# Performance work log

Measured on AMD Instinct MI355X. Metric: run time of the kernel, lower is better.

The kernel has to match this reference:

```python
import jax, jax.numpy as jnp
import numpy as np

B, L, INPUT_DIM = 4, 4096, 32
D_MODEL, N_LAYERS = 256, 2
D_STATE, D_CONV, EXPAND = 16, 4, 2
D_INNER = EXPAND * D_MODEL          # 512
DT_RANK = (D_MODEL + 15) // 16      # 16
OUTPUT_DIM, HORIZON = 32, 4
LN_EPS = 1e-5


def setup_inputs() -> dict:
    key = jax.random.key(0)
    ks = jax.random.split(key, 16)
    s = 0.02
    inp = {
        "x": jax.random.normal(ks[0], (B, L, INPUT_DIM), jnp.float32),
        "enc_w": jax.random.normal(ks[1], (D_MODEL, INPUT_DIM), jnp.float32) * s,
        "enc_b": jnp.zeros((D_MODEL,), jnp.float32),
        "in_proj_w": jax.random.normal(ks[2], (N_LAYERS, 2 * D_INNER, D_MODEL), jnp.float32) * s,
        "conv_w": jax.random.normal(ks[3], (N_LAYERS, D_INNER, D_CONV), jnp.float32) * s,
        "conv_b": jnp.zeros((N_LAYERS, D_INNER), jnp.float32),
        "xproj_w": jax.random.normal(ks[4], (N_LAYERS, DT_RANK + 2 * D_STATE, D_INNER), jnp.float32) * s,
        "dtproj_w": jax.random.normal(ks[5], (N_LAYERS, D_INNER, DT_RANK), jnp.float32) * s,
        "dtproj_b": jax.random.normal(ks[6], (N_LAYERS, D_INNER), jnp.float32) * 0.1,
        "A_log": jnp.log(jnp.tile(jnp.arange(1.0, D_STATE + 1.0, dtype=jnp.float32), (N_LAYERS, D_INNER, 1))),
        "Dp": jnp.ones((N_LAYERS, D_INNER), jnp.float32),
        "out_proj_w": jax.random.normal(ks[7], (N_LAYERS, D_MODEL, D_INNER), jnp.float32) * s,
        "ln_g": jnp.ones((D_MODEL,), jnp.float32),
        "ln_b": jnp.zeros((D_MODEL,), jnp.float32),
        "head_w": jax.random.normal(ks[8], (OUTPUT_DIM * HORIZON, D_MODEL), jnp.float32) * s,
        "head_b": jnp.zeros((OUTPUT_DIM * HORIZON,), jnp.float32),
    }
    return inp


def _mamba_block(x, in_w, cw, cb, xp_w, dt_w, dt_b, A_log, Dp, out_w):
    # x: [B, L, d_model]
    b, l, _ = x.shape
    xz = jnp.einsum("bld,ed->ble", x, in_w)            # [B, L, 2*d_inner]
    xi, res = jnp.split(xz, 2, axis=-1)
    # causal depthwise conv1d (padding=d_conv-1, truncated to L)
    xpad = jnp.pad(xi, ((0, 0), (D_CONV - 1, 0), (0, 0)))
    xi = sum(xpad[:, k:k + l, :] * cw[:, k] for k in range(D_CONV)) + cb
    xi = jax.nn.silu(xi)
    dbl = jnp.einsum("bld,ed->ble", xi, xp_w)           # [B, L, dt_rank+2*d_state]
    dt = dbl[..., :DT_RANK]
    Bm = dbl[..., DT_RANK:DT_RANK + D_STATE]            # [B, L, d_state]
    Cm = dbl[..., DT_RANK + D_STATE:]                   # [B, L, d_state]
    dt = jax.nn.softplus(jnp.einsum("blr,dr->bld", dt, dt_w) + dt_b)  # [B, L, d_inner]
    A = -jnp.exp(A_log)                                 # [d_inner, d_state]

    def step(h, ins):
        dt_t, B_t, C_t, x_t = ins                       # [B,di],[B,ds],[B,ds],[B,di]
        dA = jnp.exp(dt_t[..., None] * A)               # [B, d_inner, d_state]
        h = dA * h + (dt_t * x_t)[..., None] * B_t[:, None, :]
        y = jnp.einsum("bds,bs->bd", h, C_t)
        return h, y

    h0 = jnp.zeros((b, D_INNER, D_STATE), x.dtype)
    xs = (jnp.moveaxis(dt, 1, 0), jnp.moveaxis(Bm, 1, 0),
          jnp.moveaxis(Cm, 1, 0), jnp.moveaxis(xi, 1, 0))
    _, ys = jax.lax.scan(step, h0, xs)                  # ys: [L, B, d_inner]
    y = jnp.moveaxis(ys, 0, 1) + xi * Dp
    y = y * jax.nn.silu(res)
    return jnp.einsum("ble,de->bld", y, out_w)


def reference(x, enc_w, enc_b, in_proj_w, conv_w, conv_b, xproj_w, dtproj_w,
              dtproj_b, A_log, Dp, out_proj_w, ln_g, ln_b, head_w, head_b):
    h = jnp.einsum("bli,di->bld", x, enc_w) + enc_b     # encoder
    for i in range(N_LAYERS):
        h = h + _mamba_block(h, in_proj_w[i], conv_w[i], conv_b[i], xproj_w[i],
                             dtproj_w[i], dtproj_b[i], A_log[i], Dp[i], out_proj_w[i])
    mu = jnp.mean(h, axis=-1, keepdims=True)
    var = jnp.mean((h - mu) ** 2, axis=-1, keepdims=True)
    hn = (h - mu) * jax.lax.rsqrt(var + LN_EPS) * ln_g + ln_b
    state = hn[:, -1, :]                                # last timestep
    return jnp.einsum("bd,od->bo", state, head_w) + head_b
```

## Files before the change

### kernel.cpp

```cpp
#include <hip/hip_runtime.h>
#include <hip/hip_bf16.h>
#include <math.h>

#define BB 4
#define LL 4096
#define DM 256
#define DI 512
#define DS 16
#define NOUTK 128
#define LN_EPS 1e-5f
#define NC 128
#define CLEN (LL/NC)
#define BL (BB*LL)
#define LDB 640

typedef __attribute__((ext_vector_type(8))) short short8;
typedef __attribute__((ext_vector_type(4))) float f32x4;

__device__ __forceinline__ ushort f2bf(float f) {
    union { float f; unsigned u; } v; v.f = f;
    unsigned r = (v.u + 0x7FFF + ((v.u >> 16) & 1)) >> 16;
    return (ushort)r;
}
__device__ __forceinline__ float bf2f(ushort u) {
    union { unsigned u; float f; } v; v.u = ((unsigned)u) << 16;
    return v.f;
}

__global__ __launch_bounds__(256) void cast_bf16_kernel(
    const float* __restrict__ src, ushort* __restrict__ dst, int n)
{
    int i = blockIdx.x * 256 + threadIdx.x;
    if (i < n) dst[i] = f2bf(src[i]);
}

__global__ __launch_bounds__(256) void build_comb_kernel(
    const float* __restrict__ xpw, const float* __restrict__ dtw,
    ushort* __restrict__ dst)
{
    int i = blockIdx.x * 256 + threadIdx.x;
    int l = i / (640 * 512);
    int rem = i - l * 640 * 512;
    int row = rem >> 9, k = rem & 511;
    const float* xp = xpw + l * 48 * 512;
    const float* dw = dtw + l * 512 * 16;
    float v;
    if (row < 512) {
        v = 0.f;
        #pragma unroll
        for (int r = 0; r < 16; ++r)
            v = fmaf(dw[row * 16 + r], xp[r * 512 + k], v);
    } else if (row < 544) {
        v = xp[(row - 512 + 16) * 512 + k];
    } else v = 0.f;
    dst[i] = f2bf(v);
}

__global__ __launch_bounds__(256) void enc_kernel(
    const float* __restrict__ x, const float* __restrict__ w,
    const float* __restrict__ b, float* __restrict__ h,
    ushort* __restrict__ hbf)
{
    __shared__ float sw[256 * 33];
    __shared__ float sx[4][32];
    int tid = threadIdx.x;
    for (int i = tid; i < 256 * 8; i += 256) {
        float4 v = ((const float4*)w)[i];
        int r = i >> 3, c = (i & 7) * 4;
        sw[r * 33 + c + 0] = v.x; sw[r * 33 + c + 1] = v.y;
        sw[r * 33 + c + 2] = v.z; sw[r * 33 + c + 3] = v.w;
    }
    int row0 = blockIdx.x * 4;
    if (tid < 32) {
        for (int rr = 0; rr < 4; ++rr)
            sx[rr][tid] = x[(size_t)(row0 + rr) * 32 + tid];
    }
    __syncthreads();
    float bb = b[tid];
    #pragma unroll
    for (int rr = 0; rr < 4; ++rr) {
        float acc = bb;
        #pragma unroll
        for (int k = 0; k < 32; ++k)
            acc = fmaf(sx[rr][k], sw[tid * 33 + k], acc);
        size_t o = (size_t)(row0 + rr) * DM + tid;
        h[o] = acc;
        hbf[o] = f2bf(acc);
    }
}

template<int EPI, bool F32OUT, bool RESID, bool BF16OUT>
__global__ __launch_bounds__(256) void mfma_gemm(
    const ushort* __restrict__ A, int lda,
    const ushort* __restrict__ W,
    const float* __restrict__ bias,
    float* __restrict__ C, int ldc,
    ushort* __restrict__ Cbf, int ldcbf,
    int K)
{
    __shared__ ushort As[2][128 * 64];
    __shared__ ushort Ws[2][128 * 64];
    const int tid = threadIdx.x;

    int nwg = gridDim.x * gridDim.y;
    int wlin = blockIdx.y * gridDim.x + blockIdx.x;
    int gx = blockIdx.x, gy = blockIdx.y;
    if ((nwg & 7) == 0) {
        int q = nwg >> 3;
        int s = (wlin & 7) * q + (wlin >> 3);
        gx = s % gridDim.x;
        gy = s / gridDim.x;
    }
    const int bm = gy * 128;
    const int bn = gx * 128;
    const int wid = tid >> 6, lane = tid & 63;
    const int wrow = (wid >> 1) * 64, wcol = (wid & 1) * 64;
    const int sr = tid >> 3;
    const int sc = tid & 7;

    f32x4 acc[4][4];
    #pragma unroll
    for (int mi = 0; mi < 4; ++mi)
        #pragma unroll
        for (int ni = 0; ni < 4; ++ni)
            acc[mi][ni] = (f32x4){0.f, 0.f, 0.f, 0.f};

#define STAGE(b, k0) do {                                                     \
    _Pragma("unroll")                                                         \
    for (int it = 0; it < 4; ++it) {                                          \
        int r = it * 32 + sr;                                                 \
        int csrc = sc ^ (r & 7);                                              \
        __builtin_amdgcn_global_load_lds(                                     \
            (const __attribute__((address_space(1))) unsigned int*)           \
                (A + (size_t)(bm + r) * lda + (k0) + csrc * 8),               \
            (__attribute__((address_space(3))) unsigned int*)                 \
                (&As[b][r * 64 + sc * 8]), 16, 0, 0);                         \
    }                                                                         \
    _Pragma("unroll")                                                         \
    for (int it = 0; it < 4; ++it) {                                          \
        int r = it * 32 + sr;                                                 \
        int csrc = sc ^ (r & 7);                                              \
        __builtin_amdgcn_global_load_lds(                                     \
            (const __attribute__((address_space(1))) unsigned int*)           \
                (W + (size_t)(bn + r) * K + (k0) + csrc * 8),                 \
            (__attribute__((address_space(3))) unsigned int*)                 \
                (&Ws[b][r * 64 + sc * 8]), 16, 0, 0);                         \
    }                                                                         \
} while (0)

#define COMPUTE(b) do {                                                       \
    _Pragma("unroll")                                                         \
    for (int kk = 0; kk < 2; ++kk) {                                          \
        short8 af[4], bfr[4];                                                 \
        _Pragma("unroll")                                                     \
        for (int mi = 0; mi < 4; ++mi) {                                      \
            int r = wrow + mi * 16 + (lane & 15);                             \
            int c = (lane >> 4) + kk * 4;                                     \
            af[mi] = *(const short8*)(&As[b][r * 64 + ((c ^ (r & 7)) << 3)]); \
        }                                                                     \
        _Pragma("unroll")                                                     \
        for (int ni = 0; ni < 4; ++ni) {                                      \
            int r = wcol + ni * 16 + (lane & 15);                             \
            int c = (lane >> 4) + kk * 4;                                     \
            bfr[ni] = *(const short8*)(&Ws[b][r * 64 + ((c ^ (r & 7)) << 3)]);\
        }                                                                     \
        _Pragma("unroll")                                                     \
        for (int mi = 0; mi < 4; ++mi)                                        \
            _Pragma("unroll")                                                 \
            for (int ni = 0; ni < 4; ++ni)                                    \
                acc[mi][ni] = __builtin_amdgcn_mfma_f32_16x16x32_bf16(        \
                    af[mi], bfr[ni], acc[mi][ni], 0, 0, 0);                   \
    }                                                                         \
} while (0)

    const int nk = K >> 6;
    STAGE(0, 0);
    for (int t = 0; t < nk; t += 2) {
        __syncthreads();
        if (t + 1 < nk) STAGE(1, (t + 1) << 6);
        COMPUTE(0);
        __syncthreads();
        if (t + 2 < nk) STAGE(0, (t + 2) << 6);
        COMPUTE(1);
    }
#undef STAGE
#undef COMPUTE

    #pragma unroll
    for (int mi = 0; mi < 4; ++mi)
        #pragma unroll
        for (int ni = 0; ni < 4; ++ni) {
            int col = bn + wcol + ni * 16 + (lane & 15);
            #pragma unroll
            for (int r = 0; r < 4; ++r) {
                int row = bm + wrow + mi * 16 + (lane >> 4) * 4 + r;
                float v = acc[mi][ni][r];
                if (EPI == 1) {
                    if (col < 512) {
                        float u = v + bias[col];
                        float sp = fmaxf(u, 0.f) + __logf(1.f + __expf(-fabsf(u)));
                        Cbf[(size_t)row * ldcbf + col] = f2bf(sp);
                    } else if (col < 544) {
                        C[(size_t)row * ldc + (col - 512)] = v;
                    }
                } else {
                    if (F32OUT) {
                        float* cp = C + (size_t)row * ldc + col;
                        float vv = v;
                        if (RESID) vv += *cp;
                        *cp = vv;
                        if (BF16OUT) Cbf[(size_t)row * ldcbf + col] = f2bf(vv);
                    } else if (BF16OUT) {
                        Cbf[(size_t)row * ldcbf + col] = f2bf(v);
                    }
                }
            }
        }
}

__global__ __launch_bounds__(256) void conv_silu_kernel(
    const ushort* __restrict__ xz, const float* __restrict__ cw,
    const float* __restrict__ cb, ushort* __restrict__ xi)
{
    int idx = blockIdx.x * 256 + threadIdx.x;
    int d4 = (idx & 127) * 4;
    int bt = idx >> 7;
    int t = bt & (LL - 1);
    const ushort* base = xz + (size_t)bt * 1024 + d4;
    float acc[4];
    float4 w[4];
    #pragma unroll
    for (int j = 0; j < 4; ++j) {
        acc[j] = cb[d4 + j];
        w[j] = *(const float4*)(cw + (d4 + j) * 4);
    }
    #pragma unroll
    for (int k = 0; k < 4; ++k) {
        int back = 3 - k;
        if (t >= back) {
            ushort4 v = *(const ushort4*)(base - back * 1024);
            float wk0 = (k==0)?w[0].x:(k==1)?w[0].y:(k==2)?w[0].z:w[0].w;
            float wk1 = (k==0)?w[1].x:(k==1)?w[1].y:(k==2)?w[1].z:w[1].w;
            float wk2 = (k==0)?w[2].x:(k==1)?w[2].y:(k==2)?w[2].z:w[2].w;
            float wk3 = (k==0)?w[3].x:(k==1)?w[3].y:(k==2)?w[3].z:w[3].w;
            acc[0] = fmaf(bf2f(v.x), wk0, acc[0]);
            acc[1] = fmaf(bf2f(v.y), wk1, acc[1]);
            acc[2] = fmaf(bf2f(v.z), wk2, acc[2]);
            acc[3] = fmaf(bf2f(v.w), wk3, acc[3]);
        }
    }
    ushort4 o;
    float s0 = acc[0] / (1.f + __expf(-acc[0]));
    float s1 = acc[1] / (1.f + __expf(-acc[1]));
    float s2 = acc[2] / (1.f + __expf(-acc[2]));
    float s3 = acc[3] / (1.f + __expf(-acc[3]));
    o.x = f2bf(s0); o.y = f2bf(s1); o.z = f2bf(s2); o.w = f2bf(s3);
    *(ushort4*)(xi + (size_t)bt * 512 + d4) = o;
}

__global__ __launch_bounds__(256) void scan_phase1(
    const ushort* __restrict__ xi, const ushort* __restrict__ dtb,
    const float* __restrict__ bc,
    const float* __restrict__ alog,
    float* __restrict__ cA, float* __restrict__ cH)
{
    int d = blockIdx.z * 256 + threadIdx.x;
    int b = blockIdx.y, c = blockIdx.x;
    float Av[16];
    bool fast = true;
    #pragma unroll
    for (int s = 0; s < 16; ++s) {
        Av[s] = -__expf(alog[d * 16 + s]);
        fast = fast && (fabsf(Av[s] + (float)(s + 1)) < 1e-3f * (s + 1));
    }
    float h[16], P[16];
    #pragma unroll
    for (int s = 0; s < 16; ++s) { h[s] = 0.f; P[s] = 1.f; }
    int t0 = c * CLEN;
    if (fast) {
        float Pe = 1.f;
        for (int t = t0; t < t0 + CLEN; ++t) {
            size_t row = (size_t)b * LL + t;
            float dt = bf2f(dtb[row * 512 + d]);
            float x = bf2f(xi[row * 512 + d]);
            float dtx = dt * x;
            const float* bp = bc + row * 32;
            float e1 = __expf(-dt);
            float e2=e1*e1, e3=e2*e1, e4=e2*e2, e5=e3*e2, e6=e3*e3, e7=e4*e3, e8=e4*e4;
            float e9=e5*e4, e10=e5*e5, e11=e6*e5, e12=e6*e6, e13=e7*e6, e14=e7*e7, e15=e8*e7, e16=e8*e8;
            float pw[16] = {e1,e2,e3,e4,e5,e6,e7,e8,e9,e10,e11,e12,e13,e14,e15,e16};
            #pragma unroll
            for (int s = 0; s < 16; ++s)
                h[s] = fmaf(pw[s], h[s], dtx * bp[s]);
            Pe *= e1;
        }
        float p1=Pe, p2=p1*p1, p3=p2*p1, p4=p2*p2, p5=p3*p2, p6=p3*p3, p7=p4*p3, p8=p4*p4;
        float p9=p5*p4, p10=p5*p5, p11=p6*p5, p12=p6*p6, p13=p7*p6, p14=p7*p7, p15=p8*p7, p16=p8*p8;
        float pp[16] = {p1,p2,p3,p4,p5,p6,p7,p8,p9,p10,p11,p12,p13,p14,p15,p16};
        #pragma unroll
        for (int s = 0; s < 16; ++s) P[s] = pp[s];
    } else {
        for (int t = t0; t < t0 + CLEN; ++t) {
            size_t row = (size_t)b * LL + t;
            float dt = bf2f(dtb[row * 512 + d]);
            float x = bf2f(xi[row * 512 + d]);
            float dtx = dt * x;
            const float* bp = bc + row * 32;
            #pragma unroll
            for (int s = 0; s < 16; ++s) {
                float dA = __expf(dt * Av[s]);
                h[s] = fmaf(dA, h[s], dtx * bp[s]);
                P[s] *= dA;
            }
        }
    }
    size_t base = (((size_t)b * DI + d) * NC + c) * 16;
    #pragma unroll
    for (int q = 0; q < 4; ++q) {
        *(float4*)(cA + base + q*4) = *(float4*)&P[q*4];
        *(float4*)(cH + base + q*4) = *(float4*)&h[q*4];
    }
}

__global__ __launch_bounds__(256) void scan_phase2(
    const float* __restrict__ cA, float* __restrict__ cH)
{
    int idx = blockIdx.x * 256 + threadIdx.x;
    int s = idx & 15;
    int bd = idx >> 4;
    size_t base = (size_t)bd * NC * 16 + s;
    float init = 0.f;
    for (int c = 0; c < NC; ++c) {
        size_t o = base + (size_t)c * 16;
        float a = cA[o], hh = cH[o];
        cH[o] = init;
        init = fmaf(a, init, hh);
    }
}

__global__ __launch_bounds__(256) void scan_phase3(
    const ushort* __restrict__ xz,
    ushort* __restrict__ xi,
    const ushort* __restrict__ dtb,
    const float* __restrict__ bc,
    const float* __restrict__ alog,
    const float* __restrict__ Dp,
    const float* __restrict__ cH,
    int c0)
{
    int d = blockIdx.z * 256 + threadIdx.x;
    int b = blockIdx.y;
    int c = blockIdx.x + c0;
    float Av[16];
    bool fast = true;
    #pragma unroll
    for (int s = 0; s < 16; ++s) {
        Av[s] = -__expf(alog[d * 16 + s]);
        fast = fast && (fabsf(Av[s] + (float)(s + 1)) < 1e-3f * (s + 1));
    }
    float h[16];
    size_t cbase = (((size_t)b * DI + d) * NC + c) * 16;
    #pragma unroll
    for (int q = 0; q < 4; ++q)
        *(float4*)&h[q*4] = *(const float4*)(cH + cbase + q*4);
    float Dd = Dp[d];
    int t0 = c * CLEN;
    if (fast) {
        for (int t = t0; t < t0 + CLEN; ++t) {
            size_t row = (size_t)b * LL + t;
            float dt = bf2f(dtb[row * 512 + d]);
            float x = bf2f(xi[row * 512 + d]);
            float dtx = dt * x;
            const float* bp = bc + row * 32;
            const float* cp = bc + row * 32 + 16;
            float e1 = __expf(-dt);
            float e2=e1*e1, e3=e2*e1, e4=e2*e2, e5=e3*e2, e6=e3*e3, e7=e4*e3, e8=e4*e4;
            float e9=e5*e4, e10=e5*e5, e11=e6*e5, e12=e6*e6, e13=e7*e6, e14=e7*e7, e15=e8*e7, e16=e8*e8;
            float pw[16] = {e1,e2,e3,e4,e5,e6,e7,e8,e9,e10,e11,e12,e13,e14,e15,e16};
            float y = 0.f;
            #pragma unroll
            for (int s = 0; s < 16; ++s) {
                h[s] = fmaf(pw[s], h[s], dtx * bp[s]);
                y = fmaf(h[s], cp[s], y);
            }
            float res = bf2f(xz[row * 1024 + 512 + d]);
            float g = (y + x * Dd) * (res / (1.f + __expf(-res)));
            xi[row * 512 + d] = f2bf(g);
        }
    } else {
        for (int t = t0; t < t0 + CLEN; ++t) {
            size_t row = (size_t)b * LL + t;
            float dt = bf2f(dtb[row * 512 + d]);
            float x = bf2f(xi[row * 512 + d]);
            float dtx = dt * x;
            const float* bp = bc + row * 32;
            const float* cp = bc + row * 32 + 16;
            float y = 0.f;
            #pragma unroll
            for (int s = 0; s < 16; ++s) {
                float dA = __expf(dt * Av[s]);
                h[s] = fmaf(dA, h[s], dtx * bp[s]);
                y = fmaf(h[s], cp[s], y);
            }
            float res = bf2f(xz[row * 1024 + 512 + d]);
            float g = (y + x * Dd) * (res / (1.f + __expf(-res)));
            xi[row * 512 + d] = f2bf(g);
        }
    }
}

__global__ __launch_bounds__(256) void out_proj_last_kernel(
    const ushort* __restrict__ xi, const float* __restrict__ W,
    float* __restrict__ h)
{
    int b = blockIdx.x, n = threadIdx.x;
    __shared__ float sy[DI];
    const ushort* yrow = xi + ((size_t)b * LL + (LL - 1)) * DI;
    for (int k = threadIdx.x; k < DI; k += 256) sy[k] = bf2f(yrow[k]);
    __syncthreads();
    const float* wr = W + (size_t)n * DI;
    float acc = 0.f;
    for (int k = 0; k < DI; k += 4) {
        float4 wv = *(const float4*)(wr + k);
        acc = fmaf(sy[k+0], wv.x, acc);
        acc = fmaf(sy[k+1], wv.y, acc);
        acc = fmaf(sy[k+2], wv.z, acc);
        acc = fmaf(sy[k+3], wv.w, acc);
    }
    h[((size_t)b * LL + (LL - 1)) * DM + n] += acc;
}

__global__ __launch_bounds__(256) void ln_head_kernel(
    const float* __restrict__ h, const float* __restrict__ lng,
    const float* __restrict__ lnb, const float* __restrict__ hw,
    const float* __restrict__ hb, float* __restrict__ out)
{
    int b = blockIdx.x, tid = threadIdx.x;
    __shared__ float sh[DM];
    __shared__ float r1[4], r2[4];
    float v = h[((size_t)b * LL + (LL - 1)) * DM + tid];
    float s = v;
    #pragma unroll
    for (int o = 32; o >= 1; o >>= 1) s += __shfl_down(s, o);
    if ((tid & 63) == 0) r1[tid >> 6] = s;
    __syncthreads();
    float mu = (r1[0] + r1[1] + r1[2] + r1[3]) * (1.f / 256.f);
    float dv = v - mu;
    float q = dv * dv;
    #pragma unroll
    for (int o = 32; o >= 1; o >>= 1) q += __shfl_down(q, o);
    if ((tid & 63) == 0) r2[tid >> 6] = q;
    __syncthreads();
    float var = (r2[0] + r2[1] + r2[2] + r2[3]) * (1.f / 256.f);
    sh[tid] = dv * rsqrtf(var + LN_EPS) * lng[tid] + lnb[tid];
    __syncthreads();
    if (tid < NOUTK) {
        const float* wr = hw + (size_t)tid * DM;
        float acc = hb[tid];
        for (int d2 = 0; d2 < DM; d2 += 4) {
            float4 wv = *(const float4*)(wr + d2);
            acc = fmaf(sh[d2+0], wv.x, acc);
            acc = fmaf(sh[d2+1], wv.y, acc);
            acc = fmaf(sh[d2+2], wv.z, acc);
            acc = fmaf(sh[d2+3], wv.w, acc);
        }
        out[b * NOUTK + tid] = acc;
    }
}

extern "C" void kernel_launch(void* const* d_in, const int* in_sizes, int n_in,
                              void* d_out, int out_size, void* d_ws, size_t ws_size,
                              hipStream_t stream)
{
    const float* x    = (const float*)d_in[0];
    const float* encw = (const float*)d_in[1];
    const float* encb = (const float*)d_in[2];
    const float* inw  = (const float*)d_in[3];
    const float* cw   = (const float*)d_in[4];
    const float* cb   = (const float*)d_in[5];
    const float* xpw  = (const float*)d_in[6];
    const float* dtw  = (const float*)d_in[7];
    const float* dtb  = (const float*)d_in[8];
    const float* alog = (const float*)d_in[9];
    const float* Dp   = (const float*)d_in[10];
    const float* opw  = (const float*)d_in[11];
    const float* lng  = (const float*)d_in[12];
    const float* lnb  = (const float*)d_in[13];
    const float* hw   = (const float*)d_in[14];
    const float* hb   = (const float*)d_in[15];
    float* out = (float*)d_out;

    float* ws   = (float*)d_ws;
    float* h    = ws;
    float* bc   = h   + (size_t)BL * DM;
    float* cA   = bc  + (size_t)BL * 32;
    float* cH   = cA  + (size_t)BB * DI * NC * DS;
    ushort* h_bf    = (ushort*)(cH + (size_t)BB * DI * NC * DS);
    ushort* xz_bf   = h_bf  + (size_t)BL * DM;
    ushort* xi_bf   = xz_bf + (size_t)BL * 1024;
    ushort* dt_bf   = xi_bf + (size_t)BL * DI;
    ushort* inw_bf  = dt_bf + (size_t)BL * DI;
    ushort* opw_bf  = inw_bf + 2 * 1024 * DM;
    ushort* comb_bf = opw_bf + 2 * DM * DI;

    dim3 blk(256, 1, 1);

    cast_bf16_kernel<<<dim3((2*1024*DM)/256), blk, 0, stream>>>(inw, inw_bf, 2*1024*DM);
    cast_bf16_kernel<<<dim3((2*DM*DI)/256), blk, 0, stream>>>(opw, opw_bf, 2*DM*DI);
    build_comb_kernel<<<dim3((2*640*512)/256), blk, 0, stream>>>(xpw, dtw, comb_bf);

    enc_kernel<<<dim3(BL/4), blk, 0, stream>>>(x, encw, encb, h, h_bf);

    for (int l = 0; l < 2; ++l) {
        mfma_gemm<0,false,false,true><<<dim3(1024/128, BL/128), blk, 0, stream>>>(
            h_bf, DM, inw_bf + (size_t)l * 1024 * DM, nullptr,
            nullptr, 0, xz_bf, 1024, DM);
        conv_silu_kernel<<<dim3(BL * 128 / 256), blk, 0, stream>>>(
            xz_bf, cw + l * DI * 4, cb + l * DI, xi_bf);
        mfma_gemm<1,false,false,false><<<dim3(LDB/128, BL/128), blk, 0, stream>>>(
            xi_bf, DI, comb_bf + (size_t)l * LDB * DI, dtb + l * DI,
            bc, 32, dt_bf, 512, DI);
        scan_phase1<<<dim3(NC, BB, 2), blk, 0, stream>>>(
            xi_bf, dt_bf, bc, alog + (size_t)l * DI * 16, cA, cH);
        scan_phase2<<<dim3(BB * DI * DS / 256), blk, 0, stream>>>(cA, cH);
        if (l == 0) {
            scan_phase3<<<dim3(NC, BB, 2), blk, 0, stream>>>(
                xz_bf, xi_bf, dt_bf, bc, alog + (size_t)l * DI * 16,
                Dp + l * DI, cH, 0);
            mfma_gemm<0,true,true,true><<<dim3(DM/128, BL/128), blk, 0, stream>>>(
                xi_bf, DI, opw_bf + (size_t)l * DM * DI, nullptr,
                h, DM, h_bf, DM, DI);
        } else {
            scan_phase3<<<dim3(1, BB, 2), blk, 0, stream>>>(
                xz_bf, xi_bf, dt_bf, bc, alog + (size_t)l * DI * 16,
                Dp + l * DI, cH, NC - 1);
            out_proj_last_kernel<<<dim3(BB), blk, 0, stream>>>(
                xi_bf, opw + (size_t)l * DM * DI, h);
        }
    }

    ln_head_kernel<<<dim3(BB), blk, 0, stream>>>(h, lng, lnb, hw, hb, out);
}
```

Measured before the change: 375.1 us.

## Shrink GEMM M-tile, single-barrier prefetch pipeline, parallelize scan phase2

The MFMA GEMM M-tile drops from 128 to 64 rows, and the kernel gets launch bounds for four waves per SIMD, so there are twice as many workgroups and higher occupancy. The K loop now issues the next stage's global-to-LDS loads and waits with an explicit vmcnt rather than a full sync. scan_phase2 moves from one thread serially walking all 128 chunks per (b,d,s) to 16 threads per state, each combining 8 chunks, with a shuffle-based prefix scan across them. The trade-offs are less weight reuse per tile and a hand-written vmcnt count that must stay in step with the number of loads issued.

Result: no change. 375.0 us (-0.0%).

```diff
diff --git a/kernel.cpp b/kernel.cpp
--- a/kernel.cpp
+++ b/kernel.cpp
@@ -90,7 +90,7 @@
 }
 
 template<int EPI, bool F32OUT, bool RESID, bool BF16OUT>
-__global__ __launch_bounds__(256) void mfma_gemm(
+__global__ __launch_bounds__(256, 4) void mfma_gemm(
     const ushort* __restrict__ A, int lda,
     const ushort* __restrict__ W,
     const float* __restrict__ bias,
@@ -98,8 +98,8 @@
     ushort* __restrict__ Cbf, int ldcbf,
     int K)
 {
-    __shared__ ushort As[2][128 * 64];
-    __shared__ ushort Ws[2][128 * 64];
+    __shared__ __align__(16) ushort As[2][64 * 64];
+    __shared__ __align__(16) ushort Ws[2][128 * 64];
     const int tid = threadIdx.x;
 
     int nwg = gridDim.x * gridDim.y;
@@ -111,30 +111,30 @@
         gx = s % gridDim.x;
         gy = s / gridDim.x;
     }
-    const int bm = gy * 128;
+    const int bm = gy * 64;
     const int bn = gx * 128;
     const int wid = tid >> 6, lane = tid & 63;
-    const int wrow = (wid >> 1) * 64, wcol = (wid & 1) * 64;
+    const int wrow = (wid >> 1) * 32, wcol = (wid & 1) * 64;
     const int sr = tid >> 3;
     const int sc = tid & 7;
 
-    f32x4 acc[4][4];
-    #pragma unroll
-    for (int mi = 0; mi < 4; ++mi)
+    f32x4 acc[2][4];
+    #pragma unroll
+    for (int mi = 0; mi < 2; ++mi)
         #pragma unroll
         for (int ni = 0; ni < 4; ++ni)
             acc[mi][ni] = (f32x4){0.f, 0.f, 0.f, 0.f};
 
-#define STAGE(b, k0) do {                                                     \
+#define STAGE(buf, k0) do {                                                   \
     _Pragma("unroll")                                                         \
-    for (int it = 0; it < 4; ++it) {                                          \
+    for (int it = 0; it < 2; ++it) {                                          \
         int r = it * 32 + sr;                                                 \
         int csrc = sc ^ (r & 7);                                              \
         __builtin_amdgcn_global_load_lds(                                     \
             (const __attribute__((address_space(1))) unsigned int*)           \
                 (A + (size_t)(bm + r) * lda + (k0) + csrc * 8),               \
             (__attribute__((address_space(3))) unsigned int*)                 \
-                (&As[b][r * 64 + sc * 8]), 16, 0, 0);                         \
+                (&As[buf][r * 64 + sc * 8]), 16, 0, 0);                       \
     }                                                                         \
     _Pragma("unroll")                                                         \
     for (int it = 0; it < 4; ++it) {                                          \
@@ -144,28 +144,28 @@
             (const __attribute__((address_space(1))) unsigned int*)           \
                 (W + (size_t)(bn + r) * K + (k0) + csrc * 8),                 \
             (__attribute__((address_space(3))) unsigned int*)                 \
-                (&Ws[b][r * 64 + sc * 8]), 16, 0, 0);                         \
+                (&Ws[buf][r * 64 + sc * 8]), 16, 0, 0);                       \
     }                                                                         \
 } while (0)
 
-#define COMPUTE(b) do {                                                       \
+#define COMPUTE(buf) do {                                                     \
     _Pragma("unroll")                                                         \
     for (int kk = 0; kk < 2; ++kk) {                                          \
-        short8 af[4], bfr[4];                                                 \
+        short8 af[2], bfr[4];                                                 \
         _Pragma("unroll")                                                     \
-        for (int mi = 0; mi < 4; ++mi) {                                      \
+        for (int mi = 0; mi < 2; ++mi) {                                      \
             int r = wrow + mi * 16 + (lane & 15);                             \
             int c = (lane >> 4) + kk * 4;                                     \
-            af[mi] = *(const short8*)(&As[b][r * 64 + ((c ^ (r & 7)) << 3)]); \
+            af[mi] = *(const short8*)(&As[buf][r * 64 + ((c ^ (r & 7)) << 3)]);\
         }                                                                     \
         _Pragma("unroll")                                                     \
         for (int ni = 0; ni < 4; ++ni) {                                      \
             int r = wcol + ni * 16 + (lane & 15);                             \
             int c = (lane >> 4) + kk * 4;                                     \
-            bfr[ni] = *(const short8*)(&Ws[b][r * 64 + ((c ^ (r & 7)) << 3)]);\
+            bfr[ni] = *(const short8*)(&Ws[buf][r * 64 + ((c ^ (r & 7)) << 3)]);\
         }                                                                     \
         _Pragma("unroll")                                                     \
-        for (int mi = 0; mi < 4; ++mi)                                        \
+        for (int mi = 0; mi < 2; ++mi)                                        \
             _Pragma("unroll")                                                 \
             for (int ni = 0; ni < 4; ++ni)                                    \
                 acc[mi][ni] = __builtin_amdgcn_mfma_f32_16x16x32_bf16(        \
@@ -175,19 +175,24 @@
 
     const int nk = K >> 6;
     STAGE(0, 0);
-    for (int t = 0; t < nk; t += 2) {
-        __syncthreads();
-        if (t + 1 < nk) STAGE(1, (t + 1) << 6);
-        COMPUTE(0);
-        __syncthreads();
-        if (t + 2 < nk) STAGE(0, (t + 2) << 6);
-        COMPUTE(1);
+    for (int t = 0; t < nk; ++t) {
+        if (t + 1 < nk) {
+            STAGE((t + 1) & 1, (t + 1) << 6);
+            asm volatile("s_waitcnt vmcnt(6)" ::: "memory");
+        } else {
+            asm volatile("s_waitcnt vmcnt(0)" ::: "memory");
+        }
+        __builtin_amdgcn_s_barrier();
+        asm volatile("" ::: "memory");
+        COMPUTE(t & 1);
+        asm volatile("" ::: "memory");
+        __builtin_amdgcn_s_barrier();
     }
 #undef STAGE
 #undef COMPUTE
 
     #pragma unroll
-    for (int mi = 0; mi < 4; ++mi)
+    for (int mi = 0; mi < 2; ++mi)
         #pragma unroll
         for (int ni = 0; ni < 4; ++ni) {
             int col = bn + wcol + ni * 16 + (lane & 15);
@@ -325,16 +330,36 @@
 __global__ __launch_bounds__(256) void scan_phase2(
     const float* __restrict__ cA, float* __restrict__ cH)
 {
-    int idx = blockIdx.x * 256 + threadIdx.x;
-    int s = idx & 15;
-    int bd = idx >> 4;
+    int bd = blockIdx.x;
+    int tid = threadIdx.x;
+    int s = tid >> 4;
+    int g = tid & 15;
     size_t base = (size_t)bd * NC * 16 + s;
-    float init = 0.f;
-    for (int c = 0; c < NC; ++c) {
-        size_t o = base + (size_t)c * 16;
-        float a = cA[o], hh = cH[o];
+    float a8[8], h8[8];
+    #pragma unroll
+    for (int j = 0; j < 8; ++j) {
+        size_t o = base + (size_t)(g * 8 + j) * 16;
+        a8[j] = cA[o]; h8[j] = cH[o];
+    }
+    float A = 1.f, H = 0.f;
+    #pragma unroll
+    for (int j = 0; j < 8; ++j) {
+        H = fmaf(a8[j], H, h8[j]);
+        A *= a8[j];
+    }
+    #pragma unroll
+    for (int off = 1; off < 16; off <<= 1) {
+        float Ap = __shfl_up(A, off, 16);
+        float Hp = __shfl_up(H, off, 16);
+        if (g >= off) { H = fmaf(A, Hp, H); A *= Ap; }
+    }
+    float init = __shfl_up(H, 1, 16);
+    if (g == 0) init = 0.f;
+    #pragma unroll
+    for (int j = 0; j < 8; ++j) {
+        size_t o = base + (size_t)(g * 8 + j) * 16;
         cH[o] = init;
-        init = fmaf(a, init, hh);
+        init = fmaf(a8[j], init, h8[j]);
     }
 }
 
@@ -512,22 +537,22 @@
     enc_kernel<<<dim3(BL/4), blk, 0, stream>>>(x, encw, encb, h, h_bf);
 
     for (int l = 0; l < 2; ++l) {
-        mfma_gemm<0,false,false,true><<<dim3(1024/128, BL/128), blk, 0, stream>>>(
+        mfma_gemm<0,false,false,true><<<dim3(1024/128, BL/64), blk, 0, stream>>>(
             h_bf, DM, inw_bf + (size_t)l * 1024 * DM, nullptr,
             nullptr, 0, xz_bf, 1024, DM);
         conv_silu_kernel<<<dim3(BL * 128 / 256), blk, 0, stream>>>(
             xz_bf, cw + l * DI * 4, cb + l * DI, xi_bf);
-        mfma_gemm<1,false,false,false><<<dim3(LDB/128, BL/128), blk, 0, stream>>>(
+        mfma_gemm<1,false,false,false><<<dim3(LDB/128, BL/64), blk, 0, stream>>>(
             xi_bf, DI, comb_bf + (size_t)l * LDB * DI, dtb + l * DI,
             bc, 32, dt_bf, 512, DI);
         scan_phase1<<<dim3(NC, BB, 2), blk, 0, stream>>>(
             xi_bf, dt_bf, bc, alog + (size_t)l * DI * 16, cA, cH);
-        scan_phase2<<<dim3(BB * DI * DS / 256), blk, 0, stream>>>(cA, cH);
+        scan_phase2<<<dim3(BB * DI), blk, 0, stream>>>(cA, cH);
         if (l == 0) {
             scan_phase3<<<dim3(NC, BB, 2), blk, 0, stream>>>(
                 xz_bf, xi_bf, dt_bf, bc, alog + (size_t)l * DI * 16,
                 Dp + l * DI, cH, 0);
-            mfma_gemm<0,true,true,true><<<dim3(DM/128, BL/128), blk, 0, stream>>>(
+            mfma_gemm<0,true,true,true><<<dim3(DM/128, BL/64), blk, 0, stream>>>(
                 xi_bf, DI, opw_bf + (size_t)l * DM * DI, nullptr,
                 h, DM, h_bf, DM, DI);
         } else {
```
